# Kernel optimization log

Measured on AMD Instinct MI355X. Metric: run time of the kernel, lower is better.

The kernel has to match this reference:

```python
import jax, jax.numpy as jnp
import numpy as np

B, T, C, H = 4, 4096, 1024, 64

def setup_inputs() -> dict:
    key = jax.random.key(0)
    k1, k2, k3, k4 = jax.random.split(key, 4)
    x = jax.random.normal(k1, (B, T, C), dtype=jnp.float32)
    # nn.Linear(C, H, bias=False): y = x @ W^T with W [H, C]; store as [C, H] for x @ W
    Wq = jax.random.normal(k2, (C, H), dtype=jnp.float32) * (C ** -0.5)
    Wk = jax.random.normal(k3, (C, H), dtype=jnp.float32) * (C ** -0.5)
    Wv = jax.random.normal(k4, (C, H), dtype=jnp.float32) * (C ** -0.5)
    return {"x": x, "Wq": Wq, "Wk": Wk, "Wv": Wv}

def reference(x, Wq, Wk, Wv):
    # Manual causal single-head attention (dropout p=0 -> identity).
    q = x @ Wq  # [B, T, H]
    k = x @ Wk  # [B, T, H]
    v = x @ Wv  # [B, T, H]
    scale = q.shape[-1] ** -0.5
    w = jnp.einsum('bth,bsh->bts', q, k) * scale  # [B, T, T] scores
    causal = jnp.tril(jnp.ones((x.shape[1], x.shape[1]), dtype=bool))
    w = jnp.where(causal, w, -jnp.inf)
    w = jax.nn.softmax(w, axis=-1)
    out = jnp.einsum('bts,bsh->bth', w, v)  # [B, T, H]
    return out
```

## Files before the change

kernel.cpp:

```cpp
#include <hip/hip_runtime.h>
#include <math.h>

#define Bn 4
#define Tn 4096
#define Cn 1024
#define Hn 64

typedef __attribute__((ext_vector_type(8))) short short8;
typedef __attribute__((ext_vector_type(4))) float floatx4;

#define QSCALE 0.1803368801111204f

__device__ __forceinline__ unsigned short f2bf(float f) {
  union { float f; unsigned u; } v; v.f = f;
  unsigned r = v.u + 0x7FFFu + ((v.u >> 16) & 1u);
  return (unsigned short)(r >> 16);
}
__device__ __forceinline__ float bf2f(unsigned short h) {
  union { unsigned u; float f; } v; v.u = ((unsigned)h) << 16; return v.f;
}


__global__ __launch_bounds__(256) void wf_kernel(
    const float* __restrict__ Wq, const float* __restrict__ Wk,
    const float* __restrict__ Wv, unsigned short* __restrict__ Wf)
{
  __shared__ float ws[32][65];
  const int tid = threadIdx.x;
  const int m = blockIdx.x >> 5;
  const int g = blockIdx.x & 31;
  const float* W = (m == 0) ? Wq : (m == 1) ? Wk : Wv;
  const float4* src = (const float4*)(W + (size_t)g * 32 * Hn);
#pragma unroll
  for (int it = 0; it < 2; ++it) {
    int i4 = it * 256 + tid;
    float4 v = src[i4];
    int c = i4 >> 4, h = (i4 & 15) * 4;
    ws[c][h] = v.x; ws[c][h + 1] = v.y; ws[c][h + 2] = v.z; ws[c][h + 3] = v.w;
  }
  __syncthreads();
  const int nt = tid >> 6, lane = tid & 63;
  const int col = lane & 15, quad = lane >> 4;
  unsigned short t[8];
#pragma unroll
  for (int e = 0; e < 8; ++e) t[e] = f2bf(ws[quad * 8 + e][nt * 16 + col]);
  *(short8*)(Wf + ((size_t)((m * 32 + g) * 4 + nt) * 64 + lane) * 8) = *(short8*)t;
}

__global__ __launch_bounds__(256) void qkv_proj_kernel(
    const float* __restrict__ x, const unsigned short* __restrict__ Wf,
    unsigned short* __restrict__ Qf, unsigned short* __restrict__ Kf,
    unsigned short* __restrict__ Vf)
{
  __shared__ __align__(16) unsigned short xs[16896];
  unsigned short* red = xs;
  unsigned short* img = xs + 12288;

  const int tid  = threadIdx.x;
  const int wv   = tid >> 6;
  const int lane = tid & 63;
  const int col  = lane & 15;
  const int quad = lane >> 4;
  const int row0 = blockIdx.x * 16;

#pragma unroll
  for (int jj = 0; jj < 16; ++jj) {
    float4 v = *(const float4*)(x + (size_t)(row0 + jj) * Cn + wv * 256 + lane * 4);
    ushort4 u;
    u.x = f2bf(v.x); u.y = f2bf(v.y); u.z = f2bf(v.z); u.w = f2bf(v.w);
    *(ushort4*)(xs + (wv * 16 + jj) * 264 + lane * 4) = u;
  }

  floatx4 acc[3][4];
#pragma unroll
  for (int m = 0; m < 3; ++m)
#pragma unroll
    for (int nt = 0; nt < 4; ++nt) {
      acc[m][nt][0] = 0.f; acc[m][nt][1] = 0.f;
      acc[m][nt][2] = 0.f; acc[m][nt][3] = 0.f;
    }

#pragma unroll
  for (int ch = 0; ch < 8; ++ch) {
    short8 af = *(const short8*)(xs + (wv * 16 + col) * 264 + ch * 32 + quad * 8);
    const int g = wv * 8 + ch;
#pragma unroll
    for (int m = 0; m < 3; ++m)
#pragma unroll
      for (int nt = 0; nt < 4; ++nt) {
        short8 bf = *(const short8*)(Wf + ((size_t)((m * 32 + g) * 4 + nt) * 64 + lane) * 8);
        acc[m][nt] = __builtin_amdgcn_mfma_f32_16x16x32_bf16(af, bf, acc[m][nt], 0, 0, 0);
      }
  }

  __syncthreads();
#pragma unroll
  for (int m = 0; m < 3; ++m)
#pragma unroll
    for (int nt = 0; nt < 4; ++nt)
#pragma unroll
      for (int r = 0; r < 4; ++r)
        red[(((m * 4 + nt) * 4 + r) * 64 + lane) * 4 + wv] = f2bf(acc[m][nt][r]);
  __syncthreads();

#pragma unroll
  for (int pp = 0; pp < 3; ++pp) {
    const int p = wv * 3 + pp;
    const int m = p >> 2, nt = p & 3;
#pragma unroll
    for (int r = 0; r < 4; ++r) {
      ushort4 pk = *(const ushort4*)&red[((p * 4 + r) * 64 + lane) * 4];
      float v = (bf2f(pk.x) + bf2f(pk.y)) + (bf2f(pk.z) + bf2f(pk.w));
      const int tl = quad * 4 + r;
      if (m == 2) {
        img[2048 + nt * 256 + ((tl >> 3) * 16 + col) * 8 + (tl & 7)] = f2bf(v);
      } else {
        const int h = nt * 16 + col;
        const int idx = (h >> 5) * 512 + (((h >> 3) & 3)) * 128 + tl * 8 + (h & 7);
        img[m * 1024 + idx] = f2bf(m == 0 ? v * QSCALE : v);
      }
    }
  }
  __syncthreads();

  {
    const int b   = row0 >> 12;
    const int tt0 = row0 & 4095;
    const size_t qg = (size_t)(b * 256 + (tt0 >> 4)) * 1024;
    *(uint2*)(Qf + qg + tid * 4) = *(const uint2*)&img[tid * 4];
    *(uint2*)(Kf + qg + tid * 4) = *(const uint2*)&img[1024 + tid * 4];
    const int iV = tt0 >> 6, jV = (tt0 >> 5) & 1, half = (tt0 >> 4) & 1;
    const int ck = tid >> 6;
    const size_t vg = (((size_t)(b * 64 + iV) * 4 + ck) * 2 + jV) * 512 + half * 256;
    *(uint2*)(Vf + vg + (tid & 63) * 4) = *(const uint2*)&img[2048 + ck * 256 + (tid & 63) * 4];
  }
}

__global__ __launch_bounds__(256) void attn_kernel(
    const unsigned short* __restrict__ Qf, const unsigned short* __restrict__ Kf,
    const unsigned short* __restrict__ Vf, float* __restrict__ out)
{
  __shared__ __align__(16) unsigned short Ps[4][16][72];
  __shared__ __align__(16) float Om[4][16][68];
  __shared__ __align__(16) float Ml[4][16];

  const int tid  = threadIdx.x;
  const int wv   = tid >> 6;
  const int lane = tid & 63;
  const int col  = lane & 15;
  const int quad = lane >> 4;
  const int b  = blockIdx.x & 3;
  const int qt = 255 - (blockIdx.x >> 2);

  const unsigned short* Qp = Qf + (size_t)(b * 256 + qt) * 1024;
  short8 qf0 = *(const short8*)(Qp + lane * 8);
  short8 qf1 = *(const short8*)(Qp + 512 + lane * 8);

  const unsigned short* Kbase = Kf + (size_t)b * 256 * 1024;
  const unsigned short* Vbase = Vf + (size_t)b * 64 * 8 * 512;

  short8 ones;
#pragma unroll
  for (int e = 0; e < 8; ++e) ones[e] = (short)0x3F80;

  floatx4 o[4], ol;
#pragma unroll
  for (int ht = 0; ht < 4; ++ht) { o[ht][0]=0.f; o[ht][1]=0.f; o[ht][2]=0.f; o[ht][3]=0.f; }
  ol[0]=0.f; ol[1]=0.f; ol[2]=0.f; ol[3]=0.f;

  const int ntile = (qt >> 2) + 1;
  const int dtile = qt >> 2;

  for (int i = wv; i < ntile; i += 4) {
    floatx4 s[4];
#pragma unroll
    for (int kt = 0; kt < 4; ++kt) {
      const unsigned short* kp = Kbase + (size_t)(i * 4 + kt) * 1024;
      short8 kf0 = *(const short8*)(kp + lane * 8);
      short8 kf1 = *(const short8*)(kp + 512 + lane * 8);
      floatx4 c; c[0]=0.f; c[1]=0.f; c[2]=0.f; c[3]=0.f;
      c = __builtin_amdgcn_mfma_f32_16x16x32_bf16(qf0, kf0, c, 0, 0, 0);
      c = __builtin_amdgcn_mfma_f32_16x16x32_bf16(qf1, kf1, c, 0, 0, 0);
      s[kt] = c;
    }

    if (i == dtile) {
#pragma unroll
      for (int kt = 0; kt < 4; ++kt)
#pragma unroll
        for (int r = 0; r < 4; ++r)
          if (64 * i + kt * 16 + col > qt * 16 + quad * 4 + r) s[kt][r] = -INFINITY;
    }

#pragma unroll
    for (int kt = 0; kt < 4; ++kt)
#pragma unroll
      for (int r = 0; r < 4; ++r)
        s[kt][r] = __builtin_amdgcn_exp2f(s[kt][r]);

#pragma unroll
    for (int kt = 0; kt < 4; ++kt)
#pragma unroll
      for (int r = 0; r < 4; ++r)
        Ps[wv][quad * 4 + r][kt * 16 + col] = f2bf(s[kt][r]);

    short8 pf0 = *(const short8*)&Ps[wv][col][quad * 8];
    short8 pf1 = *(const short8*)&Ps[wv][col][32 + quad * 8];

#pragma unroll
    for (int ht = 0; ht < 4; ++ht) {
      const unsigned short* vp = Vbase + (size_t)((i * 4 + ht) * 2) * 512;
      short8 vf0 = *(const short8*)(vp + lane * 8);
      short8 vf1 = *(const short8*)(vp + 512 + lane * 8);
      o[ht] = __builtin_amdgcn_mfma_f32_16x16x32_bf16(pf0, vf0, o[ht], 0, 0, 0);
      o[ht] = __builtin_amdgcn_mfma_f32_16x16x32_bf16(pf1, vf1, o[ht], 0, 0, 0);
    }
    ol = __builtin_amdgcn_mfma_f32_16x16x32_bf16(pf0, ones, ol, 0, 0, 0);
    ol = __builtin_amdgcn_mfma_f32_16x16x32_bf16(pf1, ones, ol, 0, 0, 0);
  }

#pragma unroll
  for (int ht = 0; ht < 4; ++ht)
#pragma unroll
    for (int r = 0; r < 4; ++r)
      Om[wv][quad * 4 + r][ht * 16 + col] = o[ht][r];
  if (col == 0) {
#pragma unroll
    for (int r = 0; r < 4; ++r) Ml[wv][quad * 4 + r] = ol[r];
  }
  __syncthreads();

  const int rr = tid >> 4, h4 = (tid & 15) * 4;
  float L = (Ml[0][rr] + Ml[1][rr]) + (Ml[2][rr] + Ml[3][rr]);
  float4 a; a.x = 0.f; a.y = 0.f; a.z = 0.f; a.w = 0.f;
#pragma unroll
  for (int w = 0; w < 4; ++w) {
    float4 ov = *(const float4*)&Om[w][rr][h4];
    a.x += ov.x; a.y += ov.y; a.z += ov.z; a.w += ov.w;
  }
  float inv = 1.f / L;
  a.x *= inv; a.y *= inv; a.z *= inv; a.w *= inv;
  *(float4*)(out + ((size_t)b * Tn + qt * 16 + rr) * Hn + h4) = a;
}

extern "C" void kernel_launch(void* const* d_in, const int* in_sizes, int n_in,
                              void* d_out, int out_size, void* d_ws, size_t ws_size,
                              hipStream_t stream) {
  const float* x  = (const float*)d_in[0];
  const float* Wq = (const float*)d_in[1];
  const float* Wk = (const float*)d_in[2];
  const float* Wv = (const float*)d_in[3];
  float* out = (float*)d_out;

  unsigned short* Qf = (unsigned short*)d_ws;
  unsigned short* Kf = Qf + (size_t)Bn * Tn * Hn;
  unsigned short* Vf = Kf + (size_t)Bn * Tn * Hn;
  unsigned short* Wf = Vf + (size_t)Bn * Tn * Hn;

  wf_kernel<<<dim3(96), dim3(256), 0, stream>>>(Wq, Wk, Wv, Wf);
  qkv_proj_kernel<<<dim3(1024), dim3(256), 0, stream>>>(x, Wf, Qf, Kf, Vf);
  attn_kernel<<<dim3(Bn * 256), dim3(256), 0, stream>>>(Qf, Kf, Vf, out);
}
```

Before: 134.6 us.

## Double row tiles per block in projection and attention, prefetch K and V

Both the QKV projection and attention kernels now handle 32 query rows per block instead of 16. In the projection, each weight fragment feeds two MFMAs, x is read straight from global memory with no LDS staging, and the cross-wave reduction keeps the owner wave's own partial in registers. In attention, each K/V fragment is reused across two query sub-tiles, K tiles are prefetched one iteration ahead, V is loaded before the score computation, and P is packed into LDS with a cheaper rounding. The intent is to cut repeated global loads and raise MFMA density, at the cost of half as many blocks and more register pressure.

```diff
diff --git a/kernel.cpp b/kernel.cpp
--- a/kernel.cpp
+++ b/kernel.cpp
@@ -8,22 +8,27 @@
 
 typedef __attribute__((ext_vector_type(8))) short short8;
 typedef __attribute__((ext_vector_type(4))) float floatx4;
+typedef unsigned short ushort_t;
 
 #define QSCALE 0.1803368801111204f
 
-__device__ __forceinline__ unsigned short f2bf(float f) {
+__device__ __forceinline__ ushort_t f2bf(float f) {
   union { float f; unsigned u; } v; v.f = f;
   unsigned r = v.u + 0x7FFFu + ((v.u >> 16) & 1u);
-  return (unsigned short)(r >> 16);
-}
-__device__ __forceinline__ float bf2f(unsigned short h) {
+  return (ushort_t)(r >> 16);
+}
+__device__ __forceinline__ ushort_t f2bf_hu(float f) {
+  union { float f; unsigned u; } v; v.f = f;
+  return (ushort_t)((v.u + 0x8000u) >> 16);
+}
+__device__ __forceinline__ float bf2f(ushort_t h) {
   union { unsigned u; float f; } v; v.u = ((unsigned)h) << 16; return v.f;
 }
 
 
 __global__ __launch_bounds__(256) void wf_kernel(
     const float* __restrict__ Wq, const float* __restrict__ Wk,
-    const float* __restrict__ Wv, unsigned short* __restrict__ Wf)
+    const float* __restrict__ Wv, ushort_t* __restrict__ Wf)
 {
   __shared__ float ws[32][65];
   const int tid = threadIdx.x;
@@ -41,206 +46,279 @@
   __syncthreads();
   const int nt = tid >> 6, lane = tid & 63;
   const int col = lane & 15, quad = lane >> 4;
-  unsigned short t[8];
+  ushort_t t[8];
 #pragma unroll
   for (int e = 0; e < 8; ++e) t[e] = f2bf(ws[quad * 8 + e][nt * 16 + col]);
   *(short8*)(Wf + ((size_t)((m * 32 + g) * 4 + nt) * 64 + lane) * 8) = *(short8*)t;
 }
 
-__global__ __launch_bounds__(256) void qkv_proj_kernel(
-    const float* __restrict__ x, const unsigned short* __restrict__ Wf,
-    unsigned short* __restrict__ Qf, unsigned short* __restrict__ Kf,
-    unsigned short* __restrict__ Vf)
+__global__ __launch_bounds__(256, 2) void qkv_proj_kernel(
+    const float* __restrict__ x, const ushort_t* __restrict__ Wf,
+    ushort_t* __restrict__ Qf, ushort_t* __restrict__ Kf,
+    ushort_t* __restrict__ Vf)
 {
-  __shared__ __align__(16) unsigned short xs[16896];
-  unsigned short* red = xs;
-  unsigned short* img = xs + 12288;
+  __shared__ __align__(16) char smem[49152];
+  ushort_t* red = (ushort_t*)smem;
+  ushort_t* img = (ushort_t*)(smem + 36864);
 
   const int tid  = threadIdx.x;
   const int wv   = tid >> 6;
   const int lane = tid & 63;
   const int col  = lane & 15;
   const int quad = lane >> 4;
-  const int row0 = blockIdx.x * 16;
-
-#pragma unroll
-  for (int jj = 0; jj < 16; ++jj) {
-    float4 v = *(const float4*)(x + (size_t)(row0 + jj) * Cn + wv * 256 + lane * 4);
-    ushort4 u;
-    u.x = f2bf(v.x); u.y = f2bf(v.y); u.z = f2bf(v.z); u.w = f2bf(v.w);
-    *(ushort4*)(xs + (wv * 16 + jj) * 264 + lane * 4) = u;
-  }
-
-  floatx4 acc[3][4];
-#pragma unroll
-  for (int m = 0; m < 3; ++m)
-#pragma unroll
-    for (int nt = 0; nt < 4; ++nt) {
-      acc[m][nt][0] = 0.f; acc[m][nt][1] = 0.f;
-      acc[m][nt][2] = 0.f; acc[m][nt][3] = 0.f;
-    }
+  const int blk  = blockIdx.x;
+  const int row0 = blk * 32;
+
+  floatx4 acc[2][3][4];
+#pragma unroll
+  for (int sub = 0; sub < 2; ++sub)
+#pragma unroll
+    for (int m = 0; m < 3; ++m)
+#pragma unroll
+      for (int nt = 0; nt < 4; ++nt) {
+        acc[sub][m][nt][0] = 0.f; acc[sub][m][nt][1] = 0.f;
+        acc[sub][m][nt][2] = 0.f; acc[sub][m][nt][3] = 0.f;
+      }
 
 #pragma unroll
   for (int ch = 0; ch < 8; ++ch) {
-    short8 af = *(const short8*)(xs + (wv * 16 + col) * 264 + ch * 32 + quad * 8);
-    const int g = wv * 8 + ch;
+    const int gg = wv * 8 + ch;
+    short8 af[2];
+#pragma unroll
+    for (int sub = 0; sub < 2; ++sub) {
+      const float* xp = x + (size_t)(row0 + sub * 16 + col) * Cn + gg * 32 + quad * 8;
+      float4 a0 = *(const float4*)(xp);
+      float4 a1 = *(const float4*)(xp + 4);
+      ushort_t t[8];
+      t[0] = f2bf(a0.x); t[1] = f2bf(a0.y); t[2] = f2bf(a0.z); t[3] = f2bf(a0.w);
+      t[4] = f2bf(a1.x); t[5] = f2bf(a1.y); t[6] = f2bf(a1.z); t[7] = f2bf(a1.w);
+      af[sub] = *(short8*)t;
+    }
 #pragma unroll
     for (int m = 0; m < 3; ++m)
 #pragma unroll
       for (int nt = 0; nt < 4; ++nt) {
-        short8 bf = *(const short8*)(Wf + ((size_t)((m * 32 + g) * 4 + nt) * 64 + lane) * 8);
-        acc[m][nt] = __builtin_amdgcn_mfma_f32_16x16x32_bf16(af, bf, acc[m][nt], 0, 0, 0);
-      }
-  }
-
+        short8 bf = *(const short8*)(Wf + ((size_t)((m * 32 + gg) * 4 + nt) * 64 + lane) * 8);
+        acc[0][m][nt] = __builtin_amdgcn_mfma_f32_16x16x32_bf16(af[0], bf, acc[0][m][nt], 0, 0, 0);
+        acc[1][m][nt] = __builtin_amdgcn_mfma_f32_16x16x32_bf16(af[1], bf, acc[1][m][nt], 0, 0, 0);
+      }
+  }
+
+#pragma unroll
+  for (int sub = 0; sub < 2; ++sub)
+#pragma unroll
+    for (int m = 0; m < 3; ++m)
+#pragma unroll
+      for (int nt = 0; nt < 4; ++nt) {
+        const int p = (sub * 3 + m) * 4 + nt;
+        const int R = p / 6;
+        if (R != wv) {
+          const int slot = wv - (wv > R ? 1 : 0);
+          ushort4 u;
+          u.x = f2bf(acc[sub][m][nt][0]); u.y = f2bf(acc[sub][m][nt][1]);
+          u.z = f2bf(acc[sub][m][nt][2]); u.w = f2bf(acc[sub][m][nt][3]);
+          *(ushort4*)&red[(p * 64 + lane) * 12 + slot * 4] = u;
+        }
+      }
   __syncthreads();
-#pragma unroll
-  for (int m = 0; m < 3; ++m)
-#pragma unroll
-    for (int nt = 0; nt < 4; ++nt)
-#pragma unroll
-      for (int r = 0; r < 4; ++r)
-        red[(((m * 4 + nt) * 4 + r) * 64 + lane) * 4 + wv] = f2bf(acc[m][nt][r]);
-  __syncthreads();
-
-#pragma unroll
-  for (int pp = 0; pp < 3; ++pp) {
-    const int p = wv * 3 + pp;
-    const int m = p >> 2, nt = p & 3;
+
+#pragma unroll
+  for (int pp = 0; pp < 6; ++pp) {
+    const int p = wv * 6 + pp;
+    const int sub = p >= 12, mrem = p - sub * 12;
+    const int m = mrem >> 2, nt = mrem & 3;
+    const ushort_t* rp = &red[(p * 64 + lane) * 12];
+    ushort4 w0 = *(const ushort4*)(rp);
+    ushort4 w1 = *(const ushort4*)(rp + 4);
+    ushort4 w2 = *(const ushort4*)(rp + 8);
+    float v[4];
+    v[0] = acc[sub][m][nt][0] + bf2f(w0.x) + bf2f(w1.x) + bf2f(w2.x);
+    v[1] = acc[sub][m][nt][1] + bf2f(w0.y) + bf2f(w1.y) + bf2f(w2.y);
+    v[2] = acc[sub][m][nt][2] + bf2f(w0.z) + bf2f(w1.z) + bf2f(w2.z);
+    v[3] = acc[sub][m][nt][3] + bf2f(w0.w) + bf2f(w1.w) + bf2f(w2.w);
 #pragma unroll
     for (int r = 0; r < 4; ++r) {
-      ushort4 pk = *(const ushort4*)&red[((p * 4 + r) * 64 + lane) * 4];
-      float v = (bf2f(pk.x) + bf2f(pk.y)) + (bf2f(pk.z) + bf2f(pk.w));
-      const int tl = quad * 4 + r;
+      const int tlq = quad * 4 + r;
       if (m == 2) {
-        img[2048 + nt * 256 + ((tl >> 3) * 16 + col) * 8 + (tl & 7)] = f2bf(v);
+        img[4096 + nt * 512 + (tlq >> 2) * 128 + col * 8 + (tlq & 3) * 2 + sub] = f2bf(v[r]);
       } else {
         const int h = nt * 16 + col;
-        const int idx = (h >> 5) * 512 + (((h >> 3) & 3)) * 128 + tl * 8 + (h & 7);
-        img[m * 1024 + idx] = f2bf(m == 0 ? v * QSCALE : v);
+        const int idx = (h >> 5) * 512 + ((h >> 3) & 3) * 128 + tlq * 8 + (h & 7);
+        img[m * 2048 + sub * 1024 + idx] = f2bf(m == 0 ? v[r] * QSCALE : v[r]);
       }
     }
   }
   __syncthreads();
 
   {
-    const int b   = row0 >> 12;
-    const int tt0 = row0 & 4095;
-    const size_t qg = (size_t)(b * 256 + (tt0 >> 4)) * 1024;
-    *(uint2*)(Qf + qg + tid * 4) = *(const uint2*)&img[tid * 4];
-    *(uint2*)(Kf + qg + tid * 4) = *(const uint2*)&img[1024 + tid * 4];
-    const int iV = tt0 >> 6, jV = (tt0 >> 5) & 1, half = (tt0 >> 4) & 1;
-    const int ck = tid >> 6;
-    const size_t vg = (((size_t)(b * 64 + iV) * 4 + ck) * 2 + jV) * 512 + half * 256;
-    *(uint2*)(Vf + vg + (tid & 63) * 4) = *(const uint2*)&img[2048 + ck * 256 + (tid & 63) * 4];
-  }
-}
-
-__global__ __launch_bounds__(256) void attn_kernel(
-    const unsigned short* __restrict__ Qf, const unsigned short* __restrict__ Kf,
-    const unsigned short* __restrict__ Vf, float* __restrict__ out)
+    const int b = blk >> 7, g = blk & 127;
+#pragma unroll
+    for (int sub = 0; sub < 2; ++sub) {
+      const size_t qg = (size_t)(b * 256 + 2 * g + sub) * 1024 + tid * 4;
+      *(uint2*)(Qf + qg) = *(const uint2*)&img[sub * 1024 + tid * 4];
+      *(uint2*)(Kf + qg) = *(const uint2*)&img[2048 + sub * 1024 + tid * 4];
+    }
+    const int ht = tid >> 6;
+    const size_t vg = ((size_t)(b * 64 + (g >> 1)) * 8 + ht * 2 + (g & 1)) * 512 + (tid & 63) * 8;
+    *(short8*)(Vf + vg) = *(const short8*)&img[4096 + ht * 512 + (tid & 63) * 8];
+  }
+}
+
+__global__ __launch_bounds__(256, 2) void attn_kernel(
+    const ushort_t* __restrict__ Qf, const ushort_t* __restrict__ Kf,
+    const ushort_t* __restrict__ Vf, float* __restrict__ out)
 {
-  __shared__ __align__(16) unsigned short Ps[4][16][72];
-  __shared__ __align__(16) float Om[4][16][68];
-  __shared__ __align__(16) float Ml[4][16];
+  __shared__ __align__(16) ushort_t Ps[4][2][16][72];
+  __shared__ __align__(16) float Om[4][2][16][68];
+  __shared__ __align__(16) float Ml[4][2][16];
 
   const int tid  = threadIdx.x;
   const int wv   = tid >> 6;
   const int lane = tid & 63;
   const int col  = lane & 15;
   const int quad = lane >> 4;
-  const int b  = blockIdx.x & 3;
-  const int qt = 255 - (blockIdx.x >> 2);
-
-  const unsigned short* Qp = Qf + (size_t)(b * 256 + qt) * 1024;
-  short8 qf0 = *(const short8*)(Qp + lane * 8);
-  short8 qf1 = *(const short8*)(Qp + 512 + lane * 8);
-
-  const unsigned short* Kbase = Kf + (size_t)b * 256 * 1024;
-  const unsigned short* Vbase = Vf + (size_t)b * 64 * 8 * 512;
+  const int b = blockIdx.x & 3;
+  const int g = 127 - (blockIdx.x >> 2);
+
+  short8 qf[2][2];
+#pragma unroll
+  for (int sub = 0; sub < 2; ++sub)
+#pragma unroll
+    for (int half = 0; half < 2; ++half)
+      qf[sub][half] = *(const short8*)(Qf + (size_t)(b * 256 + 2 * g + sub) * 1024 + half * 512 + lane * 8);
+
+  const ushort_t* Kbase = Kf + (size_t)b * 256 * 1024;
+  const ushort_t* Vbase = Vf + (size_t)b * 64 * 8 * 512;
 
   short8 ones;
 #pragma unroll
   for (int e = 0; e < 8; ++e) ones[e] = (short)0x3F80;
 
-  floatx4 o[4], ol;
-#pragma unroll
-  for (int ht = 0; ht < 4; ++ht) { o[ht][0]=0.f; o[ht][1]=0.f; o[ht][2]=0.f; o[ht][3]=0.f; }
-  ol[0]=0.f; ol[1]=0.f; ol[2]=0.f; ol[3]=0.f;
-
-  const int ntile = (qt >> 2) + 1;
-  const int dtile = qt >> 2;
+  floatx4 o[2][4], ol[2];
+#pragma unroll
+  for (int sub = 0; sub < 2; ++sub) {
+#pragma unroll
+    for (int ht = 0; ht < 4; ++ht) { o[sub][ht][0]=0.f; o[sub][ht][1]=0.f; o[sub][ht][2]=0.f; o[sub][ht][3]=0.f; }
+    ol[sub][0]=0.f; ol[sub][1]=0.f; ol[sub][2]=0.f; ol[sub][3]=0.f;
+  }
+
+  const int ntile = ((g * 32 + 31) >> 6) + 1;
+  const int dtile = ntile - 1;
+
+  short8 kf[8], kfn[8];
+#pragma unroll
+  for (int kt = 0; kt < 4; ++kt) {
+    const ushort_t* kp = Kbase + (size_t)wv * 4096 + kt * 1024 + lane * 8;
+    kf[kt * 2]     = *(const short8*)(kp);
+    kf[kt * 2 + 1] = *(const short8*)(kp + 512);
+  }
 
   for (int i = wv; i < ntile; i += 4) {
-    floatx4 s[4];
+    short8 vf[8];
+#pragma unroll
+    for (int ht = 0; ht < 4; ++ht) {
+#pragma unroll
+      for (int kh = 0; kh < 2; ++kh)
+        vf[ht * 2 + kh] = *(const short8*)(Vbase + ((size_t)i * 8 + ht * 2 + kh) * 512 + lane * 8);
+    }
 #pragma unroll
     for (int kt = 0; kt < 4; ++kt) {
-      const unsigned short* kp = Kbase + (size_t)(i * 4 + kt) * 1024;
-      short8 kf0 = *(const short8*)(kp + lane * 8);
-      short8 kf1 = *(const short8*)(kp + 512 + lane * 8);
-      floatx4 c; c[0]=0.f; c[1]=0.f; c[2]=0.f; c[3]=0.f;
-      c = __builtin_amdgcn_mfma_f32_16x16x32_bf16(qf0, kf0, c, 0, 0, 0);
-      c = __builtin_amdgcn_mfma_f32_16x16x32_bf16(qf1, kf1, c, 0, 0, 0);
-      s[kt] = c;
-    }
+      const ushort_t* kp = Kbase + (size_t)(i + 4) * 4096 + kt * 1024 + lane * 8;
+      kfn[kt * 2]     = *(const short8*)(kp);
+      kfn[kt * 2 + 1] = *(const short8*)(kp + 512);
+    }
+
+    floatx4 s[2][4];
+#pragma unroll
+    for (int sub = 0; sub < 2; ++sub)
+#pragma unroll
+      for (int kt = 0; kt < 4; ++kt) {
+        floatx4 c; c[0]=0.f; c[1]=0.f; c[2]=0.f; c[3]=0.f;
+        c = __builtin_amdgcn_mfma_f32_16x16x32_bf16(qf[sub][0], kf[kt * 2],     c, 0, 0, 0);
+        c = __builtin_amdgcn_mfma_f32_16x16x32_bf16(qf[sub][1], kf[kt * 2 + 1], c, 0, 0, 0);
+        s[sub][kt] = c;
+      }
 
     if (i == dtile) {
 #pragma unroll
+      for (int sub = 0; sub < 2; ++sub)
+#pragma unroll
+        for (int kt = 0; kt < 4; ++kt)
+#pragma unroll
+          for (int r = 0; r < 4; ++r)
+            if (64 * i + kt * 16 + col > g * 32 + sub * 16 + quad * 4 + r)
+              s[sub][kt][r] = -INFINITY;
+    }
+
+#pragma unroll
+    for (int sub = 0; sub < 2; ++sub)
+#pragma unroll
       for (int kt = 0; kt < 4; ++kt)
 #pragma unroll
         for (int r = 0; r < 4; ++r)
-          if (64 * i + kt * 16 + col > qt * 16 + quad * 4 + r) s[kt][r] = -INFINITY;
-    }
-
-#pragma unroll
-    for (int kt = 0; kt < 4; ++kt)
+          s[sub][kt][r] = __builtin_amdgcn_exp2f(s[sub][kt][r]);
+
+#pragma unroll
+    for (int sub = 0; sub < 2; ++sub)
 #pragma unroll
       for (int r = 0; r < 4; ++r)
-        s[kt][r] = __builtin_amdgcn_exp2f(s[kt][r]);
-
-#pragma unroll
-    for (int kt = 0; kt < 4; ++kt)
+#pragma unroll
+        for (int kh = 0; kh < 2; ++kh) {
+          unsigned lo = f2bf_hu(s[sub][kh * 2][r]);
+          unsigned hi = f2bf_hu(s[sub][kh * 2 + 1][r]);
+          *(unsigned*)&Ps[wv][sub][quad * 4 + r][kh * 32 + col * 2] = (hi << 16) | lo;
+        }
+
+    short8 pf[2][2];
+#pragma unroll
+    for (int sub = 0; sub < 2; ++sub) {
+      pf[sub][0] = *(const short8*)&Ps[wv][sub][col][quad * 8];
+      pf[sub][1] = *(const short8*)&Ps[wv][sub][col][32 + quad * 8];
+    }
+
+#pragma unroll
+    for (int sub = 0; sub < 2; ++sub) {
+#pragma unroll
+      for (int ht = 0; ht < 4; ++ht) {
+        o[sub][ht] = __builtin_amdgcn_mfma_f32_16x16x32_bf16(pf[sub][0], vf[ht * 2],     o[sub][ht], 0, 0, 0);
+        o[sub][ht] = __builtin_amdgcn_mfma_f32_16x16x32_bf16(pf[sub][1], vf[ht * 2 + 1], o[sub][ht], 0, 0, 0);
+      }
+      ol[sub] = __builtin_amdgcn_mfma_f32_16x16x32_bf16(pf[sub][0], ones, ol[sub], 0, 0, 0);
+      ol[sub] = __builtin_amdgcn_mfma_f32_16x16x32_bf16(pf[sub][1], ones, ol[sub], 0, 0, 0);
+    }
+
+#pragma unroll
+    for (int u2 = 0; u2 < 8; ++u2) kf[u2] = kfn[u2];
+  }
+
+#pragma unroll
+  for (int sub = 0; sub < 2; ++sub) {
+#pragma unroll
+    for (int ht = 0; ht < 4; ++ht)
 #pragma unroll
       for (int r = 0; r < 4; ++r)
-        Ps[wv][quad * 4 + r][kt * 16 + col] = f2bf(s[kt][r]);
-
-    short8 pf0 = *(const short8*)&Ps[wv][col][quad * 8];
-    short8 pf1 = *(const short8*)&Ps[wv][col][32 + quad * 8];
-
-#pragma unroll
-    for (int ht = 0; ht < 4; ++ht) {
-      const unsigned short* vp = Vbase + (size_t)((i * 4 + ht) * 2) * 512;
-      short8 vf0 = *(const short8*)(vp + lane * 8);
-      short8 vf1 = *(const short8*)(vp + 512 + lane * 8);
-      o[ht] = __builtin_amdgcn_mfma_f32_16x16x32_bf16(pf0, vf0, o[ht], 0, 0, 0);
-      o[ht] = __builtin_amdgcn_mfma_f32_16x16x32_bf16(pf1, vf1, o[ht], 0, 0, 0);
-    }
-    ol = __builtin_amdgcn_mfma_f32_16x16x32_bf16(pf0, ones, ol, 0, 0, 0);
-    ol = __builtin_amdgcn_mfma_f32_16x16x32_bf16(pf1, ones, ol, 0, 0, 0);
-  }
-
-#pragma unroll
-  for (int ht = 0; ht < 4; ++ht)
-#pragma unroll
-    for (int r = 0; r < 4; ++r)
-      Om[wv][quad * 4 + r][ht * 16 + col] = o[ht][r];
-  if (col == 0) {
-#pragma unroll
-    for (int r = 0; r < 4; ++r) Ml[wv][quad * 4 + r] = ol[r];
+        Om[wv][sub][quad * 4 + r][ht * 16 + col] = o[sub][ht][r];
+    if (col == 0) {
+#pragma unroll
+      for (int r = 0; r < 4; ++r) Ml[wv][sub][quad * 4 + r] = ol[sub][r];
+    }
   }
   __syncthreads();
 
   const int rr = tid >> 4, h4 = (tid & 15) * 4;
-  float L = (Ml[0][rr] + Ml[1][rr]) + (Ml[2][rr] + Ml[3][rr]);
-  float4 a; a.x = 0.f; a.y = 0.f; a.z = 0.f; a.w = 0.f;
-#pragma unroll
-  for (int w = 0; w < 4; ++w) {
-    float4 ov = *(const float4*)&Om[w][rr][h4];
-    a.x += ov.x; a.y += ov.y; a.z += ov.z; a.w += ov.w;
-  }
-  float inv = 1.f / L;
-  a.x *= inv; a.y *= inv; a.z *= inv; a.w *= inv;
-  *(float4*)(out + ((size_t)b * Tn + qt * 16 + rr) * Hn + h4) = a;
+#pragma unroll
+  for (int sub = 0; sub < 2; ++sub) {
+    float L = (Ml[0][sub][rr] + Ml[1][sub][rr]) + (Ml[2][sub][rr] + Ml[3][sub][rr]);
+    float4 a; a.x = 0.f; a.y = 0.f; a.z = 0.f; a.w = 0.f;
+#pragma unroll
+    for (int w = 0; w < 4; ++w) {
+      float4 ov = *(const float4*)&Om[w][sub][rr][h4];
+      a.x += ov.x; a.y += ov.y; a.z += ov.z; a.w += ov.w;
+    }
+    float inv = 1.f / L;
+    a.x *= inv; a.y *= inv; a.z *= inv; a.w *= inv;
+    *(float4*)(out + (size_t)(b * Tn + g * 32 + sub * 16 + rr) * Hn + h4) = a;
+  }
 }
 
 extern "C" void kernel_launch(void* const* d_in, const int* in_sizes, int n_in,
@@ -252,12 +330,12 @@
   const float* Wv = (const float*)d_in[3];
   float* out = (float*)d_out;
 
-  unsigned short* Qf = (unsigned short*)d_ws;
-  unsigned short* Kf = Qf + (size_t)Bn * Tn * Hn;
-  unsigned short* Vf = Kf + (size_t)Bn * Tn * Hn;
-  unsigned short* Wf = Vf + (size_t)Bn * Tn * Hn;
+  ushort_t* Qf = (ushort_t*)d_ws;
+  ushort_t* Kf = Qf + (size_t)Bn * Tn * Hn;
+  ushort_t* Vf = Kf + (size_t)Bn * Tn * Hn;
+  ushort_t* Wf = Vf + (size_t)Bn * Tn * Hn;
 
   wf_kernel<<<dim3(96), dim3(256), 0, stream>>>(Wq, Wk, Wv, Wf);
-  qkv_proj_kernel<<<dim3(1024), dim3(256), 0, stream>>>(x, Wf, Qf, Kf, Vf);
-  attn_kernel<<<dim3(Bn * 256), dim3(256), 0, stream>>>(Qf, Kf, Vf, out);
-}
+  qkv_proj_kernel<<<dim3(512), dim3(256), 0, stream>>>(x, Wf, Qf, Kf, Vf);
+  attn_kernel<<<dim3(Bn * 128), dim3(256), 0, stream>>>(Qf, Kf, Vf, out);
+}
```

Result: slower. 245.7 us (+82.5%).
